# Performance work log

Measured on AMD Instinct MI355X. Metric: run time of the kernel, lower is better.

## Reference

```python
import jax, jax.numpy as jnp
import numpy as np

DIM = 1024
HIDDEN = 4096
NUM_EXPERTS = 8
TOP_K = 2
T = 8192


def setup_inputs() -> dict:
    key = jax.random.key(0)
    ks = jax.random.split(key, 5)
    scale = 0.02
    x = jax.random.normal(ks[0], (T, DIM), dtype=jnp.float32)
    gate_w = jax.random.normal(ks[1], (NUM_EXPERTS, DIM), dtype=jnp.float32) * scale  # Linear weight [out,in]
    w1 = jax.random.normal(ks[2], (NUM_EXPERTS, HIDDEN, DIM), dtype=jnp.float32) * scale
    w2 = jax.random.normal(ks[3], (NUM_EXPERTS, DIM, HIDDEN), dtype=jnp.float32) * scale
    w3 = jax.random.normal(ks[4], (NUM_EXPERTS, HIDDEN, DIM), dtype=jnp.float32) * scale
    return {"x": x, "gate_w": gate_w, "w1": w1, "w2": w2, "w3": w3}


def reference(x, gate_w, w1, w2, w3):
    # Router: softmax over all experts, take top-2, renormalize.
    logits = jnp.einsum('td,ed->te', x, gate_w)            # [T, E]
    probs = jax.nn.softmax(logits, axis=-1)
    topw, topi = jax.lax.top_k(probs, TOP_K)               # [T, 2]
    topw = topw / jnp.sum(topw, axis=-1, keepdims=True)
    out = jnp.zeros_like(x)
    num_experts = w1.shape[0]
    for e in range(num_experts):
        # combine weight for expert e per token (0 if not routed here)
        w_e = jnp.sum(jnp.where(topi == e, topw, 0.0), axis=-1)   # [T]
        h = jax.nn.silu(x @ w1[e].T) * (x @ w3[e].T)              # [T, HIDDEN]
        out = out + w_e[:, None] * (h @ w2[e].T)                  # [T, DIM]
    return out
```

## Files before the change

### kernel.cpp

```cpp
#include <hip/hip_runtime.h>
#include <hip/hip_bf16.h>
#include <cstdint>
#include <cstddef>

#define TK 8192
#define DIM 1024
#define HID 4096
#define NE 8

#define SK 32
#define NSUB1 (DIM / SK)
#define NSUB2 (HID / SK)
#define ASZ (512 * 8)
#define BSZ (1024 * 8)

typedef __attribute__((ext_vector_type(8))) __bf16 bfrag;
typedef __attribute__((ext_vector_type(4))) float ffrag;

static __device__ __forceinline__ ushort f2bf(float f) {
    union { float f; uint32_t u; } v; v.f = f;
    uint32_t r = (v.u + 0x7fffu + ((v.u >> 16) & 1u)) >> 16;
    return (ushort)r;
}

static __device__ __forceinline__ uint4 pack8(float4 a, float4 b) {
    union { ushort u[8]; uint4 q; } pk;
    pk.u[0] = f2bf(a.x); pk.u[1] = f2bf(a.y); pk.u[2] = f2bf(a.z); pk.u[3] = f2bf(a.w);
    pk.u[4] = f2bf(b.x); pk.u[5] = f2bf(b.y); pk.u[6] = f2bf(b.z); pk.u[7] = f2bf(b.w);
    return pk.q;
}

static __device__ __forceinline__ void gld16(const ushort* g, ushort* l) {
    __builtin_amdgcn_global_load_lds(
        (const __attribute__((address_space(1))) unsigned int*)g,
        (__attribute__((address_space(3))) unsigned int*)l, 16, 0, 0);
}

#define BARRIER() asm volatile("s_barrier" ::: "memory")
#define WAITVM(N) asm volatile("s_waitcnt vmcnt(" #N ")" ::: "memory")

#define LDSIDX(r, kc) ((((r) >> 3) << 8) + ((kc) << 6) + (((r) & 7) << 3))
#define SLOT_R(s)  ((((s) >> 5) << 3) | ((s) & 7))
#define SLOT_KC(s) (((s) >> 3) & 3)

__global__ __launch_bounds__(256) void k_cvt(const float* __restrict__ src,
                                             ushort* __restrict__ dst, int n8) {
    int i = blockIdx.x * blockDim.x + threadIdx.x;
    if (i >= n8) return;
    const float4* p = (const float4*)src + (size_t)i * 2;
    ((uint4*)dst)[i] = pack8(p[0], p[1]);
}

__global__ __launch_bounds__(256) void k_router(const float* __restrict__ x,
                                                const float* __restrict__ gw,
                                                int* __restrict__ topi, float* __restrict__ topw) {
    int t = blockIdx.x * 4 + (threadIdx.x >> 6);
    int lane = threadIdx.x & 63;
    if (t >= TK) return;
    double acc[NE];
#pragma unroll
    for (int e = 0; e < NE; ++e) acc[e] = 0.0;
    const float* xr = x + (size_t)t * DIM;
    for (int k = lane; k < DIM; k += 64) {
        double xv = (double)xr[k];
#pragma unroll
        for (int e = 0; e < NE; ++e) acc[e] += xv * (double)gw[e * DIM + k];
    }
#pragma unroll
    for (int e = 0; e < NE; ++e) {
#pragma unroll
        for (int off = 32; off > 0; off >>= 1) acc[e] += __shfl_xor(acc[e], off);
    }
    if (lane == 0) {
        int i1 = 0;
#pragma unroll
        for (int e = 1; e < NE; ++e) if (acc[e] > acc[i1]) i1 = e;
        int i2 = (i1 == 0) ? 1 : 0;
#pragma unroll
        for (int e = 0; e < NE; ++e) if (e != i1 && acc[e] > acc[i2]) i2 = e;
        double w = 1.0 / (1.0 + exp(acc[i2] - acc[i1]));
        topi[t * 2 + 0] = i1; topi[t * 2 + 1] = i2;
        topw[t * 2 + 0] = (float)w; topw[t * 2 + 1] = (float)(1.0 - w);
    }
}

__global__ void k_count(const int* __restrict__ topi, int* __restrict__ counts) {
    int i = blockIdx.x * blockDim.x + threadIdx.x;
    if (i < 2 * TK) atomicAdd(&counts[topi[i]], 1);
}

__global__ void k_scan(const int* __restrict__ counts, int* __restrict__ offs,
                       int* __restrict__ cursor, int* __restrict__ desc,
                       int* __restrict__ ndesc) {
    if (threadIdx.x == 0 && blockIdx.x == 0) {
        int s = 0, d = 0;
        for (int e = 0; e < NE; ++e) {
            offs[e] = s; cursor[e] = s;
            int tiles = (counts[e] + 127) >> 7;
            for (int t = 0; t < tiles; ++t) desc[d++] = (e << 16) | t;
            s += counts[e];
        }
        offs[NE] = s;
        ndesc[0] = d;
    }
}

__global__ void k_scatter(const int* __restrict__ topi, const float* __restrict__ topw,
                          int* __restrict__ cursor, int* __restrict__ perm, float* __restrict__ pw) {
    int t = blockIdx.x * blockDim.x + threadIdx.x;
    if (t >= TK) return;
#pragma unroll
    for (int k = 0; k < 2; ++k) {
        int e = topi[t * 2 + k];
        int pos = atomicAdd(&cursor[e], 1);
        perm[pos] = t; pw[pos] = topw[t * 2 + k];
    }
}


__global__ __launch_bounds__(512, 4) void k_ffn1(const ushort* __restrict__ xb,
                                                 const ushort* __restrict__ w1b,
                                                 const ushort* __restrict__ w3b,
                                                 const int* __restrict__ offs,
                                                 const int* __restrict__ perm,
                                                 const int* __restrict__ desc,
                                                 const int* __restrict__ ndesc_g,
                                                 ushort* __restrict__ H) {
    __shared__ ushort lA[3 * ASZ];
    __shared__ ushort lB[3 * BSZ];
    __shared__ int lTok[128];

    const int tid = threadIdx.x;
    const int lane = tid & 63, wid = tid >> 6;
    const int l15 = lane & 15, kcc = lane >> 4;
    const int wm = (wid >> 2) * 64;
    const int wn = (wid & 3) * 64;

    const int nitems = ndesc_g[0] << 5;

    const int rA = SLOT_R(tid), kcA = SLOT_KC(tid);

    bfrag a[4], b[4];
    ffrag acc[4][4];

#pragma unroll 1
    for (int w = blockIdx.x; w < nitems; w += (int)gridDim.x) {
        __syncthreads();
        const int de = desc[w >> 5];
        const int e = de >> 16, mt = de & 0xffff, nt = w & 31;
        const int m0 = offs[e] + (mt << 7);
        const int nrows = min(128, offs[e + 1] - m0);
        if (tid < 128) lTok[tid] = (tid < nrows) ? perm[m0 + tid] : perm[m0];
        __syncthreads();

        const ushort* pA = xb + (size_t)lTok[rA] * DIM + kcA * 8;
        const ushort* pBp[2];
        {
            const size_t ebase = (size_t)e * HID * DIM;
#pragma unroll
            for (int i2 = 0; i2 < 2; ++i2) {
                int s = i2 * 512 + tid;
                int r = SLOT_R(s), kc = SLOT_KC(s);
                int gg = r >> 4;
                int h = ((gg >> 1) << 4) | (r & 15);
                const ushort* wsrc = (gg & 1) ? w3b : w1b;
                pBp[i2] = wsrc + ebase + (size_t)(nt * 128 + h) * DIM + kc * 8;
            }
        }

#pragma unroll
        for (int i = 0; i < 4; ++i)
#pragma unroll
            for (int j = 0; j < 4; ++j) acc[i][j] = (ffrag)0.f;

#define STG1(buf, sx) do { if ((sx) < NSUB1) {                                   \
            gld16(pA + (sx) * SK, lA + (buf) * ASZ + (wid * 64) * 8);            \
            gld16(pBp[0] + (sx) * SK, lB + (buf) * BSZ + (wid * 64) * 8);        \
            gld16(pBp[1] + (sx) * SK, lB + (buf) * BSZ + (512 + wid * 64) * 8); } } while (0)

        STG1(0, 0);
        STG1(1, 1);
        int bc = 0, bs = 2;
#pragma unroll 1
        for (int X = 0; X < NSUB1 - 1; ++X) {
            WAITVM(3);
            BARRIER();
            const ushort* A_ = lA + bc * ASZ;
            const ushort* B_ = lB + bc * BSZ;
#pragma unroll
            for (int j = 0; j < 4; ++j) b[j] = *(const bfrag*)&B_[LDSIDX(wn + j * 16 + l15, kcc)];
#pragma unroll
            for (int i = 0; i < 4; ++i) a[i] = *(const bfrag*)&A_[LDSIDX(wm + i * 16 + l15, kcc)];
            STG1(bs, X + 2);
            __builtin_amdgcn_s_setprio(1);
#pragma unroll
            for (int i = 0; i < 4; ++i)
#pragma unroll
                for (int j = 0; j < 4; ++j)
                    acc[i][j] = __builtin_amdgcn_mfma_f32_16x16x32_bf16(a[i], b[j], acc[i][j], 0, 0, 0);
            __builtin_amdgcn_s_setprio(0);
            bc = (bc == 2) ? 0 : bc + 1;
            bs = (bs == 2) ? 0 : bs + 1;
        }
        {
            WAITVM(0);
            BARRIER();
            const ushort* A_ = lA + bc * ASZ;
            const ushort* B_ = lB + bc * BSZ;
#pragma unroll
            for (int j = 0; j < 4; ++j) b[j] = *(const bfrag*)&B_[LDSIDX(wn + j * 16 + l15, kcc)];
#pragma unroll
            for (int i = 0; i < 4; ++i) a[i] = *(const bfrag*)&A_[LDSIDX(wm + i * 16 + l15, kcc)];
            __builtin_amdgcn_s_setprio(1);
#pragma unroll
            for (int i = 0; i < 4; ++i)
#pragma unroll
                for (int j = 0; j < 4; ++j)
                    acc[i][j] = __builtin_amdgcn_mfma_f32_16x16x32_bf16(a[i], b[j], acc[i][j], 0, 0, 0);
            __builtin_amdgcn_s_setprio(0);
        }
#undef STG1

#pragma unroll
        for (int i = 0; i < 4; ++i) {
            int rbase = wm + i * 16 + ((lane >> 4) << 2);
#pragma unroll
            for (int q = 0; q < 4; ++q) {
                int rl = rbase + q;
                if (rl >= nrows) continue;
                size_t rowoff = (size_t)(m0 + rl) * HID;
#pragma unroll
                for (int jf = 0; jf < 4; jf += 2) {
                    int gg = (wn >> 4) + jf;
                    int col = nt * 128 + ((gg >> 1) << 4) + l15;
                    float h1 = acc[i][jf][q], h3 = acc[i][jf + 1][q];
                    H[rowoff + col] = f2bf((h1 / (1.f + __expf(-h1))) * h3);
                }
            }
        }
    }
}

__global__ __launch_bounds__(512, 4) void k_ffn2(const ushort* __restrict__ H,
                                                 const ushort* __restrict__ w2b,
                                                 const int* __restrict__ offs,
                                                 const int* __restrict__ perm,
                                                 const float* __restrict__ pw,
                                                 const int* __restrict__ desc,
                                                 const int* __restrict__ ndesc_g,
                                                 float* __restrict__ out) {
    __shared__ ushort lA[3 * ASZ];
    __shared__ ushort lB[3 * BSZ];
    __shared__ int lTok[128];
    __shared__ float lPw[128];

    const int tid = threadIdx.x;
    const int lane = tid & 63, wid = tid >> 6;
    const int l15 = lane & 15, kcc = lane >> 4;
    const int wm = (wid >> 2) * 64;
    const int wn = (wid & 3) * 64;

    const int nitems = ndesc_g[0] << 2;

    const int rA = SLOT_R(tid), kcA = SLOT_KC(tid);

    bfrag a[4], b[4];
    ffrag acc[4][4];

#pragma unroll 1
    for (int w = blockIdx.x; w < nitems; w += (int)gridDim.x) {
        __syncthreads();
        const int de = desc[w >> 2];
        const int e = de >> 16, mt = de & 0xffff, nt = w & 3;
        const int m0 = offs[e] + (mt << 7);
        const int nrows = min(128, offs[e + 1] - m0);
        if (tid < 128) {
            bool v = tid < nrows;
            lTok[tid] = v ? perm[m0 + tid] : 0;
            lPw[tid]  = v ? pw[m0 + tid] : 0.f;
        }
        __syncthreads();

        int posA = m0 + rA; if (posA > 2 * TK - 1) posA = 2 * TK - 1;
        const ushort* pA = H + (size_t)posA * HID + kcA * 8;
        const ushort* pBp[2];
        {
            const size_t ebase = (size_t)e * DIM * HID;
#pragma unroll
            for (int i2 = 0; i2 < 2; ++i2) {
                int s = i2 * 512 + tid;
                int r = SLOT_R(s), kc = SLOT_KC(s);
                pBp[i2] = w2b + ebase + (size_t)(nt * 256 + r) * HID + kc * 8;
            }
        }

#pragma unroll
        for (int i = 0; i < 4; ++i)
#pragma unroll
            for (int j = 0; j < 4; ++j) acc[i][j] = (ffrag)0.f;

#define STG2(buf, sx) do { if ((sx) < NSUB2) {                                   \
            gld16(pA + (sx) * SK, lA + (buf) * ASZ + (wid * 64) * 8);            \
            gld16(pBp[0] + (sx) * SK, lB + (buf) * BSZ + (wid * 64) * 8);        \
            gld16(pBp[1] + (sx) * SK, lB + (buf) * BSZ + (512 + wid * 64) * 8); } } while (0)

        STG2(0, 0);
        STG2(1, 1);
        int bc = 0, bs = 2;
#pragma unroll 1
        for (int X = 0; X < NSUB2 - 1; ++X) {
            WAITVM(3);
            BARRIER();
            const ushort* A_ = lA + bc * ASZ;
            const ushort* B_ = lB + bc * BSZ;
#pragma unroll
            for (int j = 0; j < 4; ++j) b[j] = *(const bfrag*)&B_[LDSIDX(wn + j * 16 + l15, kcc)];
#pragma unroll
            for (int i = 0; i < 4; ++i) a[i] = *(const bfrag*)&A_[LDSIDX(wm + i * 16 + l15, kcc)];
            STG2(bs, X + 2);
            __builtin_amdgcn_s_setprio(1);
#pragma unroll
            for (int i = 0; i < 4; ++i)
#pragma unroll
                for (int j = 0; j < 4; ++j)
                    acc[i][j] = __builtin_amdgcn_mfma_f32_16x16x32_bf16(a[i], b[j], acc[i][j], 0, 0, 0);
            __builtin_amdgcn_s_setprio(0);
            bc = (bc == 2) ? 0 : bc + 1;
            bs = (bs == 2) ? 0 : bs + 1;
        }
        {
            WAITVM(0);
            BARRIER();
            const ushort* A_ = lA + bc * ASZ;
            const ushort* B_ = lB + bc * BSZ;
#pragma unroll
            for (int j = 0; j < 4; ++j) b[j] = *(const bfrag*)&B_[LDSIDX(wn + j * 16 + l15, kcc)];
#pragma unroll
            for (int i = 0; i < 4; ++i) a[i] = *(const bfrag*)&A_[LDSIDX(wm + i * 16 + l15, kcc)];
            __builtin_amdgcn_s_setprio(1);
#pragma unroll
            for (int i = 0; i < 4; ++i)
#pragma unroll
                for (int j = 0; j < 4; ++j)
                    acc[i][j] = __builtin_amdgcn_mfma_f32_16x16x32_bf16(a[i], b[j], acc[i][j], 0, 0, 0);
            __builtin_amdgcn_s_setprio(0);
        }
#undef STG2

#pragma unroll
        for (int i = 0; i < 4; ++i) {
            int rbase = wm + i * 16 + ((lane >> 4) << 2);
#pragma unroll
            for (int q = 0; q < 4; ++q) {
                int rl = rbase + q;
                if (rl >= nrows) continue;
                int tok = lTok[rl];
                float wgt = lPw[rl];
                size_t rowoff = (size_t)tok * DIM;
#pragma unroll
                for (int j = 0; j < 4; ++j) {
                    int col = nt * 256 + wn + j * 16 + l15;
                    atomicAdd(&out[rowoff + col], acc[i][j][q] * wgt);
                }
            }
        }
    }
}

extern "C" void kernel_launch(void* const* d_in, const int* in_sizes, int n_in,
                              void* d_out, int out_size, void* d_ws, size_t ws_size,
                              hipStream_t stream) {
    const float* x  = (const float*)d_in[0];
    const float* gw = (const float*)d_in[1];
    const float* w1 = (const float*)d_in[2];
    const float* w2 = (const float*)d_in[3];
    const float* w3 = (const float*)d_in[4];
    float* out = (float*)d_out;

    char* ws = (char*)d_ws;
    int*    topi   = (int*)(ws + 0);
    float*  topw   = (float*)(ws + 65536);
    int*    perm   = (int*)(ws + 131072);
    float*  pw     = (float*)(ws + 196608);
    int*    counts = (int*)(ws + 262144);
    int*    offs   = (int*)(ws + 262144 + 256);
    int*    cursor = (int*)(ws + 262144 + 512);
    int*    ndesc  = (int*)(ws + 262144 + 768);
    int*    desc   = (int*)(ws + 262144 + 1024);

    const size_t OFF_XB = 524288;
    const size_t OFF_H  = OFF_XB + 16777216;
    const size_t OFF_WA = OFF_H + 134217728;
    const size_t OFF_WB = OFF_WA + 67108864;

    ushort* xb  = (ushort*)(ws + OFF_XB);
    ushort* H   = (ushort*)(ws + OFF_H);
    ushort* wA  = (ushort*)(ws + OFF_WA);
    ushort* wB  = (ushort*)(ws + OFF_WB);

    hipMemsetAsync(counts, 0, 32, stream);
    hipMemsetAsync(out, 0, (size_t)out_size * sizeof(float), stream);

    k_router<<<dim3(TK / 4), 256, 0, stream>>>(x, gw, topi, topw);
    k_count<<<dim3((2 * TK) / 256), 256, 0, stream>>>(topi, counts);
    k_scan<<<dim3(1), 64, 0, stream>>>(counts, offs, cursor, desc, ndesc);
    k_scatter<<<dim3(TK / 256), 256, 0, stream>>>(topi, topw, cursor, perm, pw);

    k_cvt<<<dim3((TK * DIM / 8) / 256), 256, 0, stream>>>(x, xb, TK * DIM / 8);
    k_cvt<<<dim3((NE * HID * DIM / 8) / 256), 256, 0, stream>>>(w1, wA, NE * HID * DIM / 8);
    k_cvt<<<dim3((NE * HID * DIM / 8) / 256), 256, 0, stream>>>(w3, wB, NE * HID * DIM / 8);

    k_ffn1<<<dim3(512), 512, 0, stream>>>(xb, wA, wB, offs, perm, desc, ndesc, H);

    k_cvt<<<dim3((NE * DIM * HID / 8) / 256), 256, 0, stream>>>(w2, wA, NE * DIM * HID / 8);

    k_ffn2<<<dim3(512), 512, 0, stream>>>(H, wA, offs, perm, pw, desc, ndesc, out);
}
```

Measured before the change: 1.003 ms.

## Shrink GEMM tiles to 128x128 with 256 threads, drop triple-buffered pipeline

Both expert FFN kernels move from 512-thread blocks with 128x256 output tiles and a 3-stage async LDS pipeline (K-step 32) to 256-thread blocks with 128x128 tiles. Each K-step of 64 is loaded synchronously and bracketed by __syncthreads, and the grid doubles to 1024 blocks. The goal is smaller LDS and more resident blocks so waves can hide latency, with finer-grained work items. The cost is losing the software prefetch overlap between loads and MFMA, lower reuse per tile, and more global traffic for A.

```diff
diff --git a/kernel.cpp b/kernel.cpp
--- a/kernel.cpp
+++ b/kernel.cpp
@@ -8,11 +8,10 @@
 #define HID 4096
 #define NE 8
 
-#define SK 32
-#define NSUB1 (DIM / SK)
-#define NSUB2 (HID / SK)
-#define ASZ (512 * 8)
-#define BSZ (1024 * 8)
+#define BK 64
+#define NIT1 (DIM / BK)
+#define NIT2 (HID / BK)
+#define HSZ 4096
 
 typedef __attribute__((ext_vector_type(8))) __bf16 bfrag;
 typedef __attribute__((ext_vector_type(4))) float ffrag;
@@ -35,9 +34,6 @@
         (const __attribute__((address_space(1))) unsigned int*)g,
         (__attribute__((address_space(3))) unsigned int*)l, 16, 0, 0);
 }
-
-#define BARRIER() asm volatile("s_barrier" ::: "memory")
-#define WAITVM(N) asm volatile("s_waitcnt vmcnt(" #N ")" ::: "memory")
 
 #define LDSIDX(r, kc) ((((r) >> 3) << 8) + ((kc) << 6) + (((r) & 7) << 3))
 #define SLOT_R(s)  ((((s) >> 5) << 3) | ((s) & 7))
@@ -118,7 +114,7 @@
 }
 
 
-__global__ __launch_bounds__(512, 4) void k_ffn1(const ushort* __restrict__ xb,
+__global__ __launch_bounds__(256, 4) void k_ffn1(const ushort* __restrict__ xb,
                                                  const ushort* __restrict__ w1b,
                                                  const ushort* __restrict__ w3b,
                                                  const int* __restrict__ offs,
@@ -126,19 +122,21 @@
                                                  const int* __restrict__ desc,
                                                  const int* __restrict__ ndesc_g,
                                                  ushort* __restrict__ H) {
-    __shared__ ushort lA[3 * ASZ];
-    __shared__ ushort lB[3 * BSZ];
+    __shared__ ushort lA[2 * HSZ];
+    __shared__ ushort lB[2 * HSZ];
     __shared__ int lTok[128];
 
     const int tid = threadIdx.x;
     const int lane = tid & 63, wid = tid >> 6;
     const int l15 = lane & 15, kcc = lane >> 4;
-    const int wm = (wid >> 2) * 64;
-    const int wn = (wid & 3) * 64;
-
-    const int nitems = ndesc_g[0] << 5;
-
-    const int rA = SLOT_R(tid), kcA = SLOT_KC(tid);
+    const int wm = (wid >> 1) * 64;
+    const int wn = (wid & 1) * 64;
+    const int gbase = wn >> 4;
+
+    const int nitems = ndesc_g[0] << 6;
+
+    const int r0 = SLOT_R(tid), k0c = SLOT_KC(tid);
+    const int r1 = SLOT_R(tid + 256), k1c = SLOT_KC(tid + 256);
 
     bfrag a[4], b[4];
     ffrag acc[4][4];
@@ -146,26 +144,24 @@
 #pragma unroll 1
     for (int w = blockIdx.x; w < nitems; w += (int)gridDim.x) {
         __syncthreads();
-        const int de = desc[w >> 5];
-        const int e = de >> 16, mt = de & 0xffff, nt = w & 31;
+        const int de = desc[w >> 6];
+        const int e = de >> 16, mt = de & 0xffff, nt = w & 63;
         const int m0 = offs[e] + (mt << 7);
         const int nrows = min(128, offs[e + 1] - m0);
         if (tid < 128) lTok[tid] = (tid < nrows) ? perm[m0 + tid] : perm[m0];
         __syncthreads();
 
-        const ushort* pA = xb + (size_t)lTok[rA] * DIM + kcA * 8;
-        const ushort* pBp[2];
+        const ushort* pA0 = xb + (size_t)lTok[r0] * DIM + k0c * 8;
+        const ushort* pA1 = xb + (size_t)lTok[r1] * DIM + k1c * 8;
+        const ushort* pB0;
+        const ushort* pB1;
         {
             const size_t ebase = (size_t)e * HID * DIM;
-#pragma unroll
-            for (int i2 = 0; i2 < 2; ++i2) {
-                int s = i2 * 512 + tid;
-                int r = SLOT_R(s), kc = SLOT_KC(s);
-                int gg = r >> 4;
-                int h = ((gg >> 1) << 4) | (r & 15);
-                const ushort* wsrc = (gg & 1) ? w3b : w1b;
-                pBp[i2] = wsrc + ebase + (size_t)(nt * 128 + h) * DIM + kc * 8;
-            }
+            int gg0 = r0 >> 4, gg1 = r1 >> 4;
+            int h0 = nt * 64 + (((gg0 >> 1) << 4) | (r0 & 15));
+            int h1 = nt * 64 + (((gg1 >> 1) << 4) | (r1 & 15));
+            pB0 = ((gg0 & 1) ? w3b : w1b) + ebase + (size_t)h0 * DIM + k0c * 8;
+            pB1 = ((gg1 & 1) ? w3b : w1b) + ebase + (size_t)h1 * DIM + k1c * 8;
         }
 
 #pragma unroll
@@ -173,53 +169,35 @@
 #pragma unroll
             for (int j = 0; j < 4; ++j) acc[i][j] = (ffrag)0.f;
 
-#define STG1(buf, sx) do { if ((sx) < NSUB1) {                                   \
-            gld16(pA + (sx) * SK, lA + (buf) * ASZ + (wid * 64) * 8);            \
-            gld16(pBp[0] + (sx) * SK, lB + (buf) * BSZ + (wid * 64) * 8);        \
-            gld16(pBp[1] + (sx) * SK, lB + (buf) * BSZ + (512 + wid * 64) * 8); } } while (0)
-
-        STG1(0, 0);
-        STG1(1, 1);
-        int bc = 0, bs = 2;
 #pragma unroll 1
-        for (int X = 0; X < NSUB1 - 1; ++X) {
-            WAITVM(3);
-            BARRIER();
-            const ushort* A_ = lA + bc * ASZ;
-            const ushort* B_ = lB + bc * BSZ;
-#pragma unroll
-            for (int j = 0; j < 4; ++j) b[j] = *(const bfrag*)&B_[LDSIDX(wn + j * 16 + l15, kcc)];
-#pragma unroll
-            for (int i = 0; i < 4; ++i) a[i] = *(const bfrag*)&A_[LDSIDX(wm + i * 16 + l15, kcc)];
-            STG1(bs, X + 2);
-            __builtin_amdgcn_s_setprio(1);
-#pragma unroll
-            for (int i = 0; i < 4; ++i)
-#pragma unroll
-                for (int j = 0; j < 4; ++j)
-                    acc[i][j] = __builtin_amdgcn_mfma_f32_16x16x32_bf16(a[i], b[j], acc[i][j], 0, 0, 0);
-            __builtin_amdgcn_s_setprio(0);
-            bc = (bc == 2) ? 0 : bc + 1;
-            bs = (bs == 2) ? 0 : bs + 1;
-        }
-        {
-            WAITVM(0);
-            BARRIER();
-            const ushort* A_ = lA + bc * ASZ;
-            const ushort* B_ = lB + bc * BSZ;
-#pragma unroll
-            for (int j = 0; j < 4; ++j) b[j] = *(const bfrag*)&B_[LDSIDX(wn + j * 16 + l15, kcc)];
-#pragma unroll
-            for (int i = 0; i < 4; ++i) a[i] = *(const bfrag*)&A_[LDSIDX(wm + i * 16 + l15, kcc)];
-            __builtin_amdgcn_s_setprio(1);
-#pragma unroll
-            for (int i = 0; i < 4; ++i)
-#pragma unroll
-                for (int j = 0; j < 4; ++j)
-                    acc[i][j] = __builtin_amdgcn_mfma_f32_16x16x32_bf16(a[i], b[j], acc[i][j], 0, 0, 0);
-            __builtin_amdgcn_s_setprio(0);
-        }
-#undef STG1
+        for (int kt = 0; kt < NIT1; ++kt) {
+            const int kb = kt * BK;
+#pragma unroll
+            for (int h = 0; h < 2; ++h) {
+                gld16(pA0 + kb + h * 32, lA + h * HSZ + (wid * 64) * 8);
+                gld16(pA1 + kb + h * 32, lA + h * HSZ + (256 + wid * 64) * 8);
+                gld16(pB0 + kb + h * 32, lB + h * HSZ + (wid * 64) * 8);
+                gld16(pB1 + kb + h * 32, lB + h * HSZ + (256 + wid * 64) * 8);
+            }
+            __syncthreads();
+#pragma unroll
+            for (int h = 0; h < 2; ++h) {
+                const ushort* A_ = lA + h * HSZ;
+                const ushort* B_ = lB + h * HSZ;
+#pragma unroll
+                for (int j = 0; j < 4; ++j) b[j] = *(const bfrag*)&B_[LDSIDX(wn + j * 16 + l15, kcc)];
+#pragma unroll
+                for (int i = 0; i < 4; ++i) a[i] = *(const bfrag*)&A_[LDSIDX(wm + i * 16 + l15, kcc)];
+                __builtin_amdgcn_s_setprio(1);
+#pragma unroll
+                for (int i = 0; i < 4; ++i)
+#pragma unroll
+                    for (int j = 0; j < 4; ++j)
+                        acc[i][j] = __builtin_amdgcn_mfma_f32_16x16x32_bf16(a[i], b[j], acc[i][j], 0, 0, 0);
+                __builtin_amdgcn_s_setprio(0);
+            }
+            __syncthreads();
+        }
 
 #pragma unroll
         for (int i = 0; i < 4; ++i) {
@@ -231,8 +209,8 @@
                 size_t rowoff = (size_t)(m0 + rl) * HID;
 #pragma unroll
                 for (int jf = 0; jf < 4; jf += 2) {
-                    int gg = (wn >> 4) + jf;
-                    int col = nt * 128 + ((gg >> 1) << 4) + l15;
+                    int gg = gbase + jf;
+                    int col = nt * 64 + ((gg >> 1) << 4) + l15;
                     float h1 = acc[i][jf][q], h3 = acc[i][jf + 1][q];
                     H[rowoff + col] = f2bf((h1 / (1.f + __expf(-h1))) * h3);
                 }
@@ -241,7 +219,7 @@
     }
 }
 
-__global__ __launch_bounds__(512, 4) void k_ffn2(const ushort* __restrict__ H,
+__global__ __launch_bounds__(256, 4) void k_ffn2(const ushort* __restrict__ H,
                                                  const ushort* __restrict__ w2b,
                                                  const int* __restrict__ offs,
                                                  const int* __restrict__ perm,
@@ -249,20 +227,21 @@
                                                  const int* __restrict__ desc,
                                                  const int* __restrict__ ndesc_g,
                                                  float* __restrict__ out) {
-    __shared__ ushort lA[3 * ASZ];
-    __shared__ ushort lB[3 * BSZ];
+    __shared__ ushort lA[2 * HSZ];
+    __shared__ ushort lB[2 * HSZ];
     __shared__ int lTok[128];
     __shared__ float lPw[128];
 
     const int tid = threadIdx.x;
     const int lane = tid & 63, wid = tid >> 6;
     const int l15 = lane & 15, kcc = lane >> 4;
-    const int wm = (wid >> 2) * 64;
-    const int wn = (wid & 3) * 64;
-
-    const int nitems = ndesc_g[0] << 2;
-
-    const int rA = SLOT_R(tid), kcA = SLOT_KC(tid);
+    const int wm = (wid >> 1) * 64;
+    const int wn = (wid & 1) * 64;
+
+    const int nitems = ndesc_g[0] << 3;
+
+    const int r0 = SLOT_R(tid), k0c = SLOT_KC(tid);
+    const int r1 = SLOT_R(tid + 256), k1c = SLOT_KC(tid + 256);
 
     bfrag a[4], b[4];
     ffrag acc[4][4];
@@ -270,8 +249,8 @@
 #pragma unroll 1
     for (int w = blockIdx.x; w < nitems; w += (int)gridDim.x) {
         __syncthreads();
-        const int de = desc[w >> 2];
-        const int e = de >> 16, mt = de & 0xffff, nt = w & 3;
+        const int de = desc[w >> 3];
+        const int e = de >> 16, mt = de & 0xffff, nt = w & 7;
         const int m0 = offs[e] + (mt << 7);
         const int nrows = min(128, offs[e + 1] - m0);
         if (tid < 128) {
@@ -281,71 +260,48 @@
         }
         __syncthreads();
 
-        int posA = m0 + rA; if (posA > 2 * TK - 1) posA = 2 * TK - 1;
-        const ushort* pA = H + (size_t)posA * HID + kcA * 8;
-        const ushort* pBp[2];
-        {
-            const size_t ebase = (size_t)e * DIM * HID;
-#pragma unroll
-            for (int i2 = 0; i2 < 2; ++i2) {
-                int s = i2 * 512 + tid;
-                int r = SLOT_R(s), kc = SLOT_KC(s);
-                pBp[i2] = w2b + ebase + (size_t)(nt * 256 + r) * HID + kc * 8;
-            }
-        }
+        int p0 = m0 + r0; if (p0 > 2 * TK - 1) p0 = 2 * TK - 1;
+        int p1 = m0 + r1; if (p1 > 2 * TK - 1) p1 = 2 * TK - 1;
+        const ushort* pA0 = H + (size_t)p0 * HID + k0c * 8;
+        const ushort* pA1 = H + (size_t)p1 * HID + k1c * 8;
+        const size_t ebase = (size_t)e * DIM * HID;
+        const ushort* pB0 = w2b + ebase + (size_t)(nt * 128 + r0) * HID + k0c * 8;
+        const ushort* pB1 = w2b + ebase + (size_t)(nt * 128 + r1) * HID + k1c * 8;
 
 #pragma unroll
         for (int i = 0; i < 4; ++i)
 #pragma unroll
             for (int j = 0; j < 4; ++j) acc[i][j] = (ffrag)0.f;
 
-#define STG2(buf, sx) do { if ((sx) < NSUB2) {                                   \
-            gld16(pA + (sx) * SK, lA + (buf) * ASZ + (wid * 64) * 8);            \
-            gld16(pBp[0] + (sx) * SK, lB + (buf) * BSZ + (wid * 64) * 8);        \
-            gld16(pBp[1] + (sx) * SK, lB + (buf) * BSZ + (512 + wid * 64) * 8); } } while (0)
-
-        STG2(0, 0);
-        STG2(1, 1);
-        int bc = 0, bs = 2;
 #pragma unroll 1
-        for (int X = 0; X < NSUB2 - 1; ++X) {
-            WAITVM(3);
-            BARRIER();
-            const ushort* A_ = lA + bc * ASZ;
-            const ushort* B_ = lB + bc * BSZ;
-#pragma unroll
-            for (int j = 0; j < 4; ++j) b[j] = *(const bfrag*)&B_[LDSIDX(wn + j * 16 + l15, kcc)];
-#pragma unroll
-            for (int i = 0; i < 4; ++i) a[i] = *(const bfrag*)&A_[LDSIDX(wm + i * 16 + l15, kcc)];
-            STG2(bs, X + 2);
-            __builtin_amdgcn_s_setprio(1);
-#pragma unroll
-            for (int i = 0; i < 4; ++i)
-#pragma unroll
-                for (int j = 0; j < 4; ++j)
-                    acc[i][j] = __builtin_amdgcn_mfma_f32_16x16x32_bf16(a[i], b[j], acc[i][j], 0, 0, 0);
-            __builtin_amdgcn_s_setprio(0);
-            bc = (bc == 2) ? 0 : bc + 1;
-            bs = (bs == 2) ? 0 : bs + 1;
-        }
-        {
-            WAITVM(0);
-            BARRIER();
-            const ushort* A_ = lA + bc * ASZ;
-            const ushort* B_ = lB + bc * BSZ;
-#pragma unroll
-            for (int j = 0; j < 4; ++j) b[j] = *(const bfrag*)&B_[LDSIDX(wn + j * 16 + l15, kcc)];
-#pragma unroll
-            for (int i = 0; i < 4; ++i) a[i] = *(const bfrag*)&A_[LDSIDX(wm + i * 16 + l15, kcc)];
-            __builtin_amdgcn_s_setprio(1);
-#pragma unroll
-            for (int i = 0; i < 4; ++i)
-#pragma unroll
-                for (int j = 0; j < 4; ++j)
-                    acc[i][j] = __builtin_amdgcn_mfma_f32_16x16x32_bf16(a[i], b[j], acc[i][j], 0, 0, 0);
-            __builtin_amdgcn_s_setprio(0);
-        }
-#undef STG2
+        for (int kt = 0; kt < NIT2; ++kt) {
+            const int kb = kt * BK;
+#pragma unroll
+            for (int h = 0; h < 2; ++h) {
+                gld16(pA0 + kb + h * 32, lA + h * HSZ + (wid * 64) * 8);
+                gld16(pA1 + kb + h * 32, lA + h * HSZ + (256 + wid * 64) * 8);
+                gld16(pB0 + kb + h * 32, lB + h * HSZ + (wid * 64) * 8);
+                gld16(pB1 + kb + h * 32, lB + h * HSZ + (256 + wid * 64) * 8);
+            }
+            __syncthreads();
+#pragma unroll
+            for (int h = 0; h < 2; ++h) {
+                const ushort* A_ = lA + h * HSZ;
+                const ushort* B_ = lB + h * HSZ;
+#pragma unroll
+                for (int j = 0; j < 4; ++j) b[j] = *(const bfrag*)&B_[LDSIDX(wn + j * 16 + l15, kcc)];
+#pragma unroll
+                for (int i = 0; i < 4; ++i) a[i] = *(const bfrag*)&A_[LDSIDX(wm + i * 16 + l15, kcc)];
+                __builtin_amdgcn_s_setprio(1);
+#pragma unroll
+                for (int i = 0; i < 4; ++i)
+#pragma unroll
+                    for (int j = 0; j < 4; ++j)
+                        acc[i][j] = __builtin_amdgcn_mfma_f32_16x16x32_bf16(a[i], b[j], acc[i][j], 0, 0, 0);
+                __builtin_amdgcn_s_setprio(0);
+            }
+            __syncthreads();
+        }
 
 #pragma unroll
         for (int i = 0; i < 4; ++i) {
@@ -359,7 +315,7 @@
                 size_t rowoff = (size_t)tok * DIM;
 #pragma unroll
                 for (int j = 0; j < 4; ++j) {
-                    int col = nt * 256 + wn + j * 16 + l15;
+                    int col = nt * 128 + wn + j * 16 + l15;
                     atomicAdd(&out[rowoff + col], acc[i][j][q] * wgt);
                 }
             }
@@ -410,9 +366,9 @@
     k_cvt<<<dim3((NE * HID * DIM / 8) / 256), 256, 0, stream>>>(w1, wA, NE * HID * DIM / 8);
     k_cvt<<<dim3((NE * HID * DIM / 8) / 256), 256, 0, stream>>>(w3, wB, NE * HID * DIM / 8);
 
-    k_ffn1<<<dim3(512), 512, 0, stream>>>(xb, wA, wB, offs, perm, desc, ndesc, H);
+    k_ffn1<<<dim3(1024), 256, 0, stream>>>(xb, wA, wB, offs, perm, desc, ndesc, H);
 
     k_cvt<<<dim3((NE * DIM * HID / 8) / 256), 256, 0, stream>>>(w2, wA, NE * DIM * HID / 8);
 
-    k_ffn2<<<dim3(512), 512, 0, stream>>>(H, wA, offs, perm, pw, desc, ndesc, out);
-}
+    k_ffn2<<<dim3(1024), 256, 0, stream>>>(H, wA, offs, perm, pw, desc, ndesc, out);
+}
```

After: 1.185 ms. +18.2%, slower.
